# Kernel optimization log

Measured on AMD Instinct MI355X. Metric: run time of the kernel, lower is better.

## Reference

```python
import jax, jax.numpy as jnp
import numpy as np

B, S, E, H = 4, 2048, 1024, 16
HD = E // H  # per-head dim = 64


def setup_inputs() -> dict:
    key = jax.random.key(0)
    ks = jax.random.split(key, 12)
    scale = 1.0 / np.sqrt(E)
    inp = {
        "q": jax.random.normal(ks[0], (B, S, E), jnp.float32),
        "k": jax.random.normal(ks[1], (B, S, E), jnp.float32),
        "v": jax.random.normal(ks[2], (B, S, E), jnp.float32),
        # causal mask: True = masked out (matches torch masked_fill_ semantics)
        "mask": jnp.triu(jnp.ones((S, S), jnp.bool_), k=1)[None, None, :, :],
        "Wq": jax.random.normal(ks[3], (E, E), jnp.float32) * scale,
        "bq": jnp.zeros((E,), jnp.float32),
        "Wk": jax.random.normal(ks[4], (E, E), jnp.float32) * scale,
        "bk": jnp.zeros((E,), jnp.float32),
        "Wv": jax.random.normal(ks[5], (E, E), jnp.float32) * scale,
        "bv": jnp.zeros((E,), jnp.float32),
        "Wo": jax.random.normal(ks[6], (E, E), jnp.float32) * scale,
        "bo": jnp.zeros((E,), jnp.float32),
    }
    return inp


def reference(q, k, v, mask, Wq, bq, Wk, bk, Wv, bv, Wo, bo):
    # QKV projections (nn.Linear: x @ W.T + b)
    query = q @ Wq.T + bq
    key_ = k @ Wk.T + bk
    value = v @ Wv.T + bv
    # split heads: [B, S, E] -> [B, H, S, HD]
    mq = query.reshape(B, S, H, HD).transpose(0, 2, 1, 3)
    mk = key_.reshape(B, S, H, HD).transpose(0, 2, 1, 3)
    mv = value.reshape(B, S, H, HD).transpose(0, 2, 1, 3)
    # scaled dot-product attention with explicit score matrix [B, H, S, S]
    scores = jnp.einsum("bhqd,bhkd->bhqk", mq, mk) / jnp.sqrt(jnp.float32(HD))
    scores = jnp.where(mask, -jnp.inf, scores)
    probs = jax.nn.softmax(scores, axis=-1)
    ctx = jnp.einsum("bhqk,bhkd->bhqd", probs, mv)
    # merge heads and output projection
    ctx = ctx.transpose(0, 2, 1, 3).reshape(B, S, E)
    return ctx @ Wo.T + bo
```

## Files before the change

kernel.cpp:

```cpp
#include <hip/hip_runtime.h>
#include <hip/hip_bf16.h>
#include <math.h>

#define B_ 4
#define S_ 2048
#define E_ 1024
#define H_ 16
#define HD_ 64
#define NEG_ (-1e30f)
#define SC2_ 0.18033688f
#define EXP2(x) __builtin_amdgcn_exp2f(x)

typedef __bf16 bf16x8 __attribute__((ext_vector_type(8)));
typedef __bf16 bf16x4 __attribute__((ext_vector_type(4)));
typedef float f32x4 __attribute__((ext_vector_type(4)));

#define MFMA(a, b, c) __builtin_amdgcn_mfma_f32_16x16x32_bf16((a), (b), (c), 0, 0, 0)

#define GLDS16(gp, lp)                                                        \
  __builtin_amdgcn_global_load_lds(                                           \
      (const __attribute__((address_space(1))) void*)(gp),                    \
      (__attribute__((address_space(3))) void*)(lp), 16, 0, 0)

__device__ __forceinline__ bf16x8 cvt8(const float4 a, const float4 b) {
  bf16x8 r;
  r[0] = (__bf16)a.x; r[1] = (__bf16)a.y; r[2] = (__bf16)a.z; r[3] = (__bf16)a.w;
  r[4] = (__bf16)b.x; r[5] = (__bf16)b.y; r[6] = (__bf16)b.z; r[7] = (__bf16)b.w;
  return r;
}

__device__ __forceinline__ f32x4 vmax4(f32x4 a, f32x4 b) {
  f32x4 r;
  r[0] = fmaxf(a[0], b[0]); r[1] = fmaxf(a[1], b[1]);
  r[2] = fmaxf(a[2], b[2]); r[3] = fmaxf(a[3], b[3]);
  return r;
}

__global__ __launch_bounds__(256)
void cvt_all_kernel(const float* __restrict__ q, const float* __restrict__ k,
                    const float* __restrict__ v,
                    const float* __restrict__ wq, const float* __restrict__ wk,
                    const float* __restrict__ wv, const float* __restrict__ wo,
                    __bf16* __restrict__ q16, __bf16* __restrict__ k16,
                    __bf16* __restrict__ v16,
                    __bf16* __restrict__ wqb, __bf16* __restrict__ wkb,
                    __bf16* __restrict__ wvb, __bf16* __restrict__ wob)
{
  const int bx = blockIdx.x;
  const float* src;
  __bf16* dst;
  size_t off;
  if (bx < 12288) {
    const int z = bx >> 12, r = bx & 4095;
    src = (z == 0) ? q : (z == 1) ? k : v;
    dst = (z == 0) ? q16 : (z == 1) ? k16 : v16;
    off = (size_t)r * 2048 + threadIdx.x * 8;
  } else {
    const int z = (bx - 12288) >> 9, r = (bx - 12288) & 511;
    src = (z == 0) ? wq : (z == 1) ? wk : (z == 2) ? wv : wo;
    dst = (z == 0) ? wqb : (z == 1) ? wkb : (z == 2) ? wvb : wob;
    off = (size_t)r * 2048 + threadIdx.x * 8;
  }
  const float4 a = *(const float4*)&src[off];
  const float4 b = *(const float4*)&src[off + 4];
  *(bf16x8*)&dst[off] = cvt8(a, b);
}

__global__ __launch_bounds__(256)
void cvt_w_kernel(const float* __restrict__ wq, const float* __restrict__ wk,
                  const float* __restrict__ wv, const float* __restrict__ wo,
                  __bf16* __restrict__ wqb, __bf16* __restrict__ wkb,
                  __bf16* __restrict__ wvb, __bf16* __restrict__ wob)
{
  const int y = blockIdx.y;
  const float* src = (y == 0) ? wq : (y == 1) ? wk : (y == 2) ? wv : wo;
  __bf16* dst      = (y == 0) ? wqb: (y == 1) ? wkb: (y == 2) ? wvb: wob;
  const size_t i = ((size_t)blockIdx.x * 256 + threadIdx.x) * 8;
  const float4 a = *(const float4*)&src[i];
  const float4 b = *(const float4*)&src[i + 4];
  *(bf16x8*)&dst[i] = cvt8(a, b);
}

__global__ __launch_bounds__(256)
void cvt_in_kernel(const float* __restrict__ src, __bf16* __restrict__ dst)
{
  const size_t i = ((size_t)blockIdx.x * 256 + threadIdx.x) * 8;
  const float4 a = *(const float4*)&src[i];
  const float4 b = *(const float4*)&src[i + 4];
  *(bf16x8*)&dst[i] = cvt8(a, b);
}

__global__ __launch_bounds__(256, 3)
void qkv_gemm(const __bf16* __restrict__ Aq, const __bf16* __restrict__ Ak,
              const __bf16* __restrict__ Av,
              const __bf16* __restrict__ Wqb, const __bf16* __restrict__ Wkb,
              const __bf16* __restrict__ Wvb,
              const float* __restrict__ bq, const float* __restrict__ bk,
              const float* __restrict__ bv,
              __bf16* __restrict__ Qo, __bf16* __restrict__ Ko,
              __bf16* __restrict__ Vo, int zbase)
{
  __shared__ __align__(16) __bf16 sA[128 * 64];
  __shared__ __align__(16) __bf16 sB[128 * 64];
  const int z = (int)blockIdx.z + zbase;
  const __bf16* A   = (z == 0) ? Aq  : (z == 1) ? Ak  : Av;
  const __bf16* W   = (z == 0) ? Wqb : (z == 1) ? Wkb : Wvb;
  const float* bias = (z == 0) ? bq  : (z == 1) ? bk  : bv;
  __bf16* outp      = (z == 0) ? Qo  : (z == 1) ? Ko  : Vo;

  const int t = threadIdx.x;
  const int lane = t & 63, ln = lane & 15, qd = lane >> 4;
  const int l7 = ln & 7;
  const int wv_ = t >> 6, wm = (wv_ >> 1) * 64, wn = (wv_ & 1) * 64;
  const int m0 = ((int)blockIdx.x * 8 + ((int)blockIdx.y >> 3)) * 128;
  const int n0 = ((int)blockIdx.y & 7) * 128;

  f32x4 acc[4][4] = {};
  for (int kk = 0; kk < E_; kk += 64) {
    __syncthreads();
    for (int p = 0; p < 4; ++p) {
      const int c = t + 256 * p;
      const int row = c >> 3, kc = c & 7;
      const int gcol = ((kc ^ (row & 7)) * 8);
      GLDS16(A + (size_t)(m0 + row) * E_ + kk + gcol, sA + c * 8);
      GLDS16(W + (size_t)(n0 + row) * E_ + kk + gcol, sB + c * 8);
    }
    __syncthreads();
    for (int kb2 = 0; kb2 < 2; ++kb2) {
      const int sw = ((kb2 * 4 + qd) ^ l7) * 8;
      bf16x8 af[4], bf_[4];
      for (int i = 0; i < 4; ++i)
        af[i]  = *(const bf16x8*)&sA[(wm + i * 16 + ln) * 64 + sw];
      for (int j = 0; j < 4; ++j)
        bf_[j] = *(const bf16x8*)&sB[(wn + j * 16 + ln) * 64 + sw];
      for (int i = 0; i < 4; ++i)
        for (int j = 0; j < 4; ++j)
          acc[i][j] = MFMA(af[i], bf_[j], acc[i][j]);
    }
  }

  for (int j = 0; j < 4; ++j) {
    const int n = n0 + wn + j * 16 + ln;
    const float bb = bias[n];
    const int hh = n >> 6, d = n & 63;
    for (int i = 0; i < 4; ++i) {
      for (int r2 = 0; r2 < 4; ++r2) {
        const int m = m0 + wm + i * 16 + qd * 4 + r2;
        const int b = m >> 11, s2 = m & 2047;
        float val = acc[i][j][r2] + bb;
        if (z == 0) {
          val *= SC2_;
          ((__bf16*)outp)[((size_t)(b * H_ + hh) * S_ + s2) * HD_ + d] = (__bf16)val;
        } else if (z == 1) {
          ((__bf16*)outp)[((size_t)(b * H_ + hh) * S_ + s2) * HD_ + d] = (__bf16)val;
        } else {
          ((__bf16*)outp)[((size_t)(b * H_ + hh) * HD_ + d) * S_ + s2] = (__bf16)val;
        }
      }
    }
  }
}

__global__ __launch_bounds__(256, 3)
void attn_kernel(const __bf16* __restrict__ Qg, const __bf16* __restrict__ Kg,
                 const __bf16* __restrict__ Vg, __bf16* __restrict__ Og)
{
  const int slice = blockIdx.x;
  const int h = slice & 15, b = slice >> 4;
  const int qx = 31 - (int)blockIdx.y;
  const int t = threadIdx.x;
  const int wq = t >> 6;
  const int lane = t & 63;
  const int ln = lane & 15, qd = lane >> 4;
  const int l7 = ln & 7;
  const int q0 = qx * 64;
  const size_t bh = (size_t)(b * H_ + h);

  __shared__ __align__(16) __bf16 sK[128 * 64];
  __shared__ __align__(16) __bf16 sVt[64 * 128];
  __shared__ __align__(16) __bf16 sP[64 * 136];

  bf16x8 aq[2];
  {
    const __bf16* qrowp = Qg + (bh * S_ + q0 + wq * 16 + ln) * HD_;
    aq[0] = *(const bf16x8*)&qrowp[qd * 8];
    aq[1] = *(const bf16x8*)&qrowp[32 + qd * 8];
  }

  const int myq = q0 + wq * 16 + ln;

  f32x4 o[4] = {};
  float m_prev = NEG_, l_run = 0.f;

  const int ktmax = (q0 + 63) >> 7;
  for (int kt = 0; kt <= ktmax; ++kt) {
    const int k0 = kt * 128;
    __syncthreads();
    {
      const __bf16* kbase = Kg + (bh * S_ + k0) * HD_;
      const __bf16* vbase = Vg + bh * HD_ * S_ + k0;
      for (int p = 0; p < 4; ++p) {
        const int c = t + 256 * p;
        const int kr = c >> 3, kkc = c & 7;
        GLDS16(kbase + (size_t)kr * HD_ + ((kkc ^ (kr & 7)) * 8), sK + c * 8);
        const int vr = c >> 4, vkc = c & 15;
        GLDS16(vbase + (size_t)vr * S_ + ((vkc ^ (vr & 15)) * 8), sVt + c * 8);
      }
    }
    __syncthreads();

    f32x4 sc[8] = {};
    for (int kb2 = 0; kb2 < 2; ++kb2) {
      const int sw = ((kb2 * 4 + qd) ^ l7) * 8;
      for (int nt = 0; nt < 8; ++nt) {
        bf16x8 ak8 = *(const bf16x8*)&sK[(nt * 16 + ln) * 64 + sw];
        sc[nt] = MFMA(ak8, aq[kb2], sc[nt]);
      }
    }

    if (k0 + 127 > q0) {
      const int kb = k0 + qd * 4 - myq;
      for (int nt = 0; nt < 8; ++nt)
        for (int r2 = 0; r2 < 4; ++r2)
          if (kb + nt * 16 + r2 > 0) sc[nt][r2] = NEG_;
    }

    f32x4 t0 = vmax4(vmax4(sc[0], sc[1]), vmax4(sc[2], sc[3]));
    f32x4 t1 = vmax4(vmax4(sc[4], sc[5]), vmax4(sc[6], sc[7]));
    f32x4 t2 = vmax4(t0, t1);
    float mloc = fmaxf(fmaxf(t2[0], t2[1]), fmaxf(t2[2], t2[3]));
    mloc = fmaxf(mloc, __shfl_xor(mloc, 16, 64));
    mloc = fmaxf(mloc, __shfl_xor(mloc, 32, 64));
    const float m_new = fmaxf(m_prev, mloc);
    const float alpha = EXP2(m_prev - m_new);
    m_prev = m_new;

    float rsum = 0.f;
    {
      const int pb = (wq * 16 + ln) * 136 + qd * 4;
      for (int nt = 0; nt < 8; ++nt) {
        const float p0 = EXP2(sc[nt][0] - m_new);
        const float p1 = EXP2(sc[nt][1] - m_new);
        const float p2 = EXP2(sc[nt][2] - m_new);
        const float p3 = EXP2(sc[nt][3] - m_new);
        rsum += (p0 + p1) + (p2 + p3);
        bf16x4 pk;
        pk[0] = (__bf16)p0; pk[1] = (__bf16)p1;
        pk[2] = (__bf16)p2; pk[3] = (__bf16)p3;
        *(bf16x4*)&sP[pb + nt * 16] = pk;
      }
    }
    rsum += __shfl_xor(rsum, 16, 64);
    rsum += __shfl_xor(rsum, 32, 64);
    l_run = l_run * alpha + rsum;

    float af[4];
    for (int r2 = 0; r2 < 4; ++r2)
      af[r2] = __shfl(alpha, qd * 4 + r2, 64);
    for (int dt = 0; dt < 4; ++dt)
      for (int r2 = 0; r2 < 4; ++r2)
        o[dt][r2] *= af[r2];

    for (int ks = 0; ks < 4; ++ks) {
      bf16x8 ap = *(const bf16x8*)&sP[(wq * 16 + ln) * 136 + ks * 32 + qd * 8];
      const int swv = ((ks * 4 + qd) ^ ln) * 8;
      for (int dt = 0; dt < 4; ++dt) {
        bf16x8 bv8 = *(const bf16x8*)&sVt[(dt * 16 + ln) * 128 + swv];
        o[dt] = MFMA(ap, bv8, o[dt]);
      }
    }
  }

  const float linv = 1.0f / l_run;
  float inv[4];
  for (int r2 = 0; r2 < 4; ++r2)
    inv[r2] = __shfl(linv, qd * 4 + r2, 64);
  for (int r2 = 0; r2 < 4; ++r2) {
    const int qrow = q0 + wq * 16 + qd * 4 + r2;
    for (int dt = 0; dt < 4; ++dt) {
      const int d = dt * 16 + ln;
      Og[((size_t)(b * S_ + qrow)) * E_ + h * HD_ + d] = (__bf16)(o[dt][r2] * inv[r2]);
    }
  }
}

__global__ __launch_bounds__(256, 3)
void out_gemm(const __bf16* __restrict__ A, const __bf16* __restrict__ W,
              const float* __restrict__ bias, float* __restrict__ out)
{
  __shared__ __align__(16) __bf16 sA[128 * 64];
  __shared__ __align__(16) __bf16 sB[128 * 64];
  const int t = threadIdx.x;
  const int lane = t & 63, ln = lane & 15, qd = lane >> 4;
  const int l7 = ln & 7;
  const int wv_ = t >> 6, wm = (wv_ >> 1) * 64, wn = (wv_ & 1) * 64;
  const int m0 = blockIdx.y * 128, n0 = blockIdx.x * 128;

  f32x4 acc[4][4] = {};
  for (int kk = 0; kk < E_; kk += 64) {
    __syncthreads();
    for (int p = 0; p < 4; ++p) {
      const int c = t + 256 * p;
      const int row = c >> 3, kc = c & 7;
      const int gcol = ((kc ^ (row & 7)) * 8);
      GLDS16(A + (size_t)(m0 + row) * E_ + kk + gcol, sA + c * 8);
      GLDS16(W + (size_t)(n0 + row) * E_ + kk + gcol, sB + c * 8);
    }
    __syncthreads();
    for (int kb2 = 0; kb2 < 2; ++kb2) {
      const int sw = ((kb2 * 4 + qd) ^ l7) * 8;
      bf16x8 af[4], bf_[4];
      for (int i = 0; i < 4; ++i)
        af[i]  = *(const bf16x8*)&sA[(wm + i * 16 + ln) * 64 + sw];
      for (int j = 0; j < 4; ++j)
        bf_[j] = *(const bf16x8*)&sB[(wn + j * 16 + ln) * 64 + sw];
      for (int i = 0; i < 4; ++i)
        for (int j = 0; j < 4; ++j)
          acc[i][j] = MFMA(af[i], bf_[j], acc[i][j]);
    }
  }

  for (int j = 0; j < 4; ++j) {
    const int n = n0 + wn + j * 16 + ln;
    const float bb = bias[n];
    for (int i = 0; i < 4; ++i)
      for (int r2 = 0; r2 < 4; ++r2) {
        const int m = m0 + wm + i * 16 + qd * 4 + r2;
        out[(size_t)m * E_ + n] = acc[i][j][r2] + bb;
      }
  }
}

extern "C" void kernel_launch(void* const* d_in, const int* in_sizes, int n_in,
                              void* d_out, int out_size, void* d_ws, size_t ws_size,
                              hipStream_t stream)
{
  const float* q  = (const float*)d_in[0];
  const float* k  = (const float*)d_in[1];
  const float* v  = (const float*)d_in[2];
  const float* Wq = (const float*)d_in[4];
  const float* bq = (const float*)d_in[5];
  const float* Wk = (const float*)d_in[6];
  const float* bk = (const float*)d_in[7];
  const float* Wv = (const float*)d_in[8];
  const float* bv = (const float*)d_in[9];
  const float* Wo = (const float*)d_in[10];
  const float* bo = (const float*)d_in[11];
  float* out = (float*)d_out;

  const size_t NE = (size_t)B_ * S_ * E_;
  const size_t NW = (size_t)E_ * E_;
  __bf16* Wqb = (__bf16*)d_ws;
  __bf16* Wkb = Wqb + NW;
  __bf16* Wvb = Wkb + NW;
  __bf16* Wob = Wvb + NW;
  __bf16* Qb  = Wob + NW;
  __bf16* Kb  = Qb + NE;
  __bf16* Vb  = Kb + NE;

  dim3 blk(256);
  const size_t need_fat = (4 * NW + 6 * NE) * sizeof(__bf16);
  if (ws_size >= need_fat) {
    __bf16* q16 = Vb + NE;
    __bf16* k16 = q16 + NE;
    __bf16* v16 = k16 + NE;
    __bf16* Cb  = q16;
    cvt_all_kernel<<<dim3(14336), blk, 0, stream>>>(q, k, v, Wq, Wk, Wv, Wo,
                                                    q16, k16, v16,
                                                    Wqb, Wkb, Wvb, Wob);
    qkv_gemm<<<dim3(8, 64, 3), blk, 0, stream>>>(q16, k16, v16,
                                                 Wqb, Wkb, Wvb,
                                                 bq, bk, bv, Qb, Kb, Vb, 0);
    attn_kernel<<<dim3(64, 32), blk, 0, stream>>>(Qb, Kb, Vb, Cb);
    out_gemm<<<dim3(8, 64), blk, 0, stream>>>(Cb, Wob, bo, out);
  } else {
    cvt_w_kernel<<<dim3(512, 4), blk, 0, stream>>>(Wq, Wk, Wv, Wo,
                                                   Wqb, Wkb, Wvb, Wob);
    __bf16* X16 = Vb + NE;
    __bf16* Cb  = X16;
    const float* srcs[3] = {q, k, v};
    for (int z = 0; z < 3; ++z) {
      cvt_in_kernel<<<dim3(4096), blk, 0, stream>>>(srcs[z], X16);
      qkv_gemm<<<dim3(8, 64, 1), blk, 0, stream>>>(X16, X16, X16,
                                                   Wqb, Wkb, Wvb,
                                                   bq, bk, bv, Qb, Kb, Vb, z);
    }
    attn_kernel<<<dim3(64, 32), blk, 0, stream>>>(Qb, Kb, Vb, Cb);
    out_gemm<<<dim3(8, 64), blk, 0, stream>>>(Cb, Wob, bo, out);
  }
}
```

Baseline: 332.8 us.

## Stage V transpose through LDS and add lazy softmax rescaling

The V projection epilogue now writes its tile transposed into shared memory with an XOR swizzle, then emits 16-byte coalesced stores along the sequence dimension. This replaces the scattered 2-byte strided global writes. Separately, the attention kernel skips the running-max update and the rescaling of the output accumulator whenever every lane's new block max exceeds the current max by at most 8 in log2 units. This is the lazy rescaling trick from FlashAttention-style kernels: it avoids shuffles and multiplies at the cost of exponentials bounded by 2^8 before normalization.

```diff
diff --git a/kernel.cpp b/kernel.cpp
--- a/kernel.cpp
+++ b/kernel.cpp
@@ -100,13 +100,13 @@
               __bf16* __restrict__ Qo, __bf16* __restrict__ Ko,
               __bf16* __restrict__ Vo, int zbase)
 {
-  __shared__ __align__(16) __bf16 sA[128 * 64];
-  __shared__ __align__(16) __bf16 sB[128 * 64];
+  __shared__ __align__(16) __bf16 sAB[2][128 * 64];
+  __bf16* const sA = sAB[0];
+  __bf16* const sB = sAB[1];
   const int z = (int)blockIdx.z + zbase;
   const __bf16* A   = (z == 0) ? Aq  : (z == 1) ? Ak  : Av;
   const __bf16* W   = (z == 0) ? Wqb : (z == 1) ? Wkb : Wvb;
   const float* bias = (z == 0) ? bq  : (z == 1) ? bk  : bv;
-  __bf16* outp      = (z == 0) ? Qo  : (z == 1) ? Ko  : Vo;
 
   const int t = threadIdx.x;
   const int lane = t & 63, ln = lane & 15, qd = lane >> 4;
@@ -139,24 +139,45 @@
     }
   }
 
-  for (int j = 0; j < 4; ++j) {
-    const int n = n0 + wn + j * 16 + ln;
-    const float bb = bias[n];
-    const int hh = n >> 6, d = n & 63;
-    for (int i = 0; i < 4; ++i) {
-      for (int r2 = 0; r2 < 4; ++r2) {
-        const int m = m0 + wm + i * 16 + qd * 4 + r2;
-        const int b = m >> 11, s2 = m & 2047;
-        float val = acc[i][j][r2] + bb;
-        if (z == 0) {
-          val *= SC2_;
-          ((__bf16*)outp)[((size_t)(b * H_ + hh) * S_ + s2) * HD_ + d] = (__bf16)val;
-        } else if (z == 1) {
-          ((__bf16*)outp)[((size_t)(b * H_ + hh) * S_ + s2) * HD_ + d] = (__bf16)val;
-        } else {
-          ((__bf16*)outp)[((size_t)(b * H_ + hh) * HD_ + d) * S_ + s2] = (__bf16)val;
+  if (z < 2) {
+    __bf16* outp = (z == 0) ? Qo : Ko;
+    for (int j = 0; j < 4; ++j) {
+      const int n = n0 + wn + j * 16 + ln;
+      const float bb = bias[n];
+      const int hh = n >> 6, d = n & 63;
+      for (int i = 0; i < 4; ++i) {
+        for (int r2 = 0; r2 < 4; ++r2) {
+          const int m = m0 + wm + i * 16 + qd * 4 + r2;
+          const int b = m >> 11, s2 = m & 2047;
+          float val = acc[i][j][r2] + bb;
+          if (z == 0) val *= SC2_;
+          outp[((size_t)(b * H_ + hh) * S_ + s2) * HD_ + d] = (__bf16)val;
         }
       }
+    }
+  } else {
+    __syncthreads();
+    __bf16* const sT = &sAB[0][0];
+    for (int j = 0; j < 4; ++j) {
+      const int nl = wn + j * 16 + ln;
+      const float bb = bias[n0 + nl];
+      const int rsw = (nl & 7) << 3;
+      for (int i = 0; i < 4; ++i)
+        for (int r2 = 0; r2 < 4; ++r2) {
+          const int ml = wm + i * 16 + qd * 4 + r2;
+          sT[nl * 128 + (ml ^ rsw)] = (__bf16)(acc[i][j][r2] + bb);
+        }
+    }
+    __syncthreads();
+    const int r = t >> 1, half = t & 1;
+    const int n = n0 + r, hh = n >> 6, d = n & 63;
+    const int b = m0 >> 11, s0 = m0 & 2047;
+    __bf16* dstp = Vo + ((size_t)(b * H_ + hh) * HD_ + d) * S_ + s0 + half * 64;
+    const int rsw = (r & 7) << 3;
+    for (int c8 = 0; c8 < 8; ++c8) {
+      const int mc = half * 64 + c8 * 8;
+      bf16x8 vv = *(const bf16x8*)&sT[r * 128 + (mc ^ rsw)];
+      *(bf16x8*)&dstp[c8 * 8] = vv;
     }
   }
 }
@@ -231,18 +252,28 @@
     float mloc = fmaxf(fmaxf(t2[0], t2[1]), fmaxf(t2[2], t2[3]));
     mloc = fmaxf(mloc, __shfl_xor(mloc, 16, 64));
     mloc = fmaxf(mloc, __shfl_xor(mloc, 32, 64));
-    const float m_new = fmaxf(m_prev, mloc);
-    const float alpha = EXP2(m_prev - m_new);
-    m_prev = m_new;
+
+    if (!__all(mloc - m_prev <= 8.0f)) {
+      const float m_new = fmaxf(m_prev, mloc);
+      const float alpha = EXP2(m_prev - m_new);
+      m_prev = m_new;
+      l_run *= alpha;
+      float af[4];
+      for (int r2 = 0; r2 < 4; ++r2)
+        af[r2] = __shfl(alpha, qd * 4 + r2, 64);
+      for (int dt = 0; dt < 4; ++dt)
+        for (int r2 = 0; r2 < 4; ++r2)
+          o[dt][r2] *= af[r2];
+    }
 
     float rsum = 0.f;
     {
       const int pb = (wq * 16 + ln) * 136 + qd * 4;
       for (int nt = 0; nt < 8; ++nt) {
-        const float p0 = EXP2(sc[nt][0] - m_new);
-        const float p1 = EXP2(sc[nt][1] - m_new);
-        const float p2 = EXP2(sc[nt][2] - m_new);
-        const float p3 = EXP2(sc[nt][3] - m_new);
+        const float p0 = EXP2(sc[nt][0] - m_prev);
+        const float p1 = EXP2(sc[nt][1] - m_prev);
+        const float p2 = EXP2(sc[nt][2] - m_prev);
+        const float p3 = EXP2(sc[nt][3] - m_prev);
         rsum += (p0 + p1) + (p2 + p3);
         bf16x4 pk;
         pk[0] = (__bf16)p0; pk[1] = (__bf16)p1;
@@ -252,14 +283,7 @@
     }
     rsum += __shfl_xor(rsum, 16, 64);
     rsum += __shfl_xor(rsum, 32, 64);
-    l_run = l_run * alpha + rsum;
-
-    float af[4];
-    for (int r2 = 0; r2 < 4; ++r2)
-      af[r2] = __shfl(alpha, qd * 4 + r2, 64);
-    for (int dt = 0; dt < 4; ++dt)
-      for (int r2 = 0; r2 < 4; ++r2)
-        o[dt][r2] *= af[r2];
+    l_run += rsum;
 
     for (int ks = 0; ks < 4; ++ks) {
       bf16x8 ap = *(const bf16x8*)&sP[(wq * 16 + ln) * 136 + ks * 32 + qd * 8];
```

Result: faster. 325.9 us (-2.1%).
